# Kernel tuning notes

Hardware: AMD Instinct MI355X
Metric: run time of the kernel (lower is better)

## Reference

```python
import jax, jax.numpy as jnp
import numpy as np

B, F, T, D, S = 8, 256, 512, 40, 4


def setup_inputs() -> dict:
    key = jax.random.key(0)
    k1, k2 = jax.random.split(key)
    embeddings = jax.random.normal(k1, (B, F, T, D), dtype=jnp.float32)
    assignments = jax.random.uniform(k2, (B, F, T, S), dtype=jnp.float32)
    return {"embeddings": embeddings, "assignments": assignments}


def reference(embeddings, assignments):
    b, f, t, d = embeddings.shape
    s = assignments.shape[-1]
    n = f * t
    E = embeddings.reshape(b, n, d)          # (B, N, D)
    V = assignments.reshape(b, n, s)         # (B, N, S)
    # ||VV^T - EE^T||_F^2 summed over batch, via trace identity:
    #   = ||V^T V||_F^2 - 2 ||V^T E||_F^2 + ||E^T E||_F^2
    VtV = jnp.einsum('bns,bnt->bst', V, V)   # (B, S, S)
    VtE = jnp.einsum('bns,bnd->bsd', V, E)   # (B, S, D)
    EtE = jnp.einsum('bnd,bne->bde', E, E)   # (B, D, D)
    fro_sq = jnp.sum(VtV * VtV) - 2.0 * jnp.sum(VtE * VtE) + jnp.sum(EtE * EtE)
    return fro_sq / (b * n)
```

## Files before the change

kernel.cpp:

```cpp
#include <hip/hip_runtime.h>
#include <hip/hip_bf16.h>

#define BATCHES 8
#define NROWS (256 * 512)
#define DE 40
#define SV 4
#define GP 48
#define NTILE 1536
#define ROWS_PER_BLOCK 1024
#define CHUNKS (NROWS / ROWS_PER_BLOCK)
#define RSTAGE 128
#define NSTAGES (ROWS_PER_BLOCK / RSTAGE)
#define COLBYTES 256
#define TILEBYTES (GP * COLBYTES)

typedef __attribute__((ext_vector_type(8))) short bf16x8;
typedef __attribute__((ext_vector_type(4))) float f32x4;
typedef __attribute__((ext_vector_type(2))) int i32x2;
typedef __attribute__((ext_vector_type(4))) float f4v;

__device__ __forceinline__ int pk_bf16(float lo, float hi) {
    __hip_bfloat162 h2 = __float22bfloat162_rn(float2{lo, hi});
    return *reinterpret_cast<int*>(&h2);
}

__device__ __forceinline__ float4 ldnt(const float4* p) {
    f4v v = __builtin_nontemporal_load(reinterpret_cast<const f4v*>(p));
    return make_float4(v.x, v.y, v.z, v.w);
}

__device__ __forceinline__ void bar_lgkm() {
    asm volatile("s_waitcnt lgkmcnt(0)" ::: "memory");
    __builtin_amdgcn_s_barrier();
    asm volatile("" ::: "memory");
}

struct ARegs { float4 a0, a1, a2, a3; };

__global__ __launch_bounds__(256, 4) void gram_kernel(const float* __restrict__ E,
                                                      const float* __restrict__ V,
                                                      float* __restrict__ P) {
    __shared__ __align__(16) char tb[2][TILEBYTES];

    const int tid = threadIdx.x;
    const int lane = tid & 63;
    const int wave = tid >> 6;
    const int b = blockIdx.x / CHUNKS;
    const int chunk = blockIdx.x % CHUNKS;
    const size_t row0 = (size_t)chunk * ROWS_PER_BLOCK;

    const float4* __restrict__ Eg = (const float4*)(E + (size_t)b * NROWS * DE) + row0 * 10;
    const float4* __restrict__ Vg = (const float4*)(V + (size_t)b * NROWS * SV) + row0;

    if (tid < 128) {
        const int bb = tid >> 6, off = (tid & 63) * 16;
        *(float4*)&tb[bb][44 * COLBYTES + off] = make_float4(0.f, 0.f, 0.f, 0.f);
    }

    const int cgA = tid % 11, rgA = tid / 11;
    const int cgB = (tid + 256) % 11, rgB = (tid + 256) / 11;
    const bool hasB = (tid < 96);
    const bool vA = (cgA == 10), vB = (cgB == 10);
    const int pA = vA ? 1 : 10, cA = vA ? 0 : cgA;
    const int pB = vB ? 1 : 10, cB = vB ? 0 : cgB;
    const float4* __restrict__ gA = vA ? Vg : Eg;
    const float4* __restrict__ gB = vB ? Vg : Eg;
    const int oA = 4 * rgA * pA + cA;
    const int oB = 4 * rgB * pB + cB;

    f32x4 acc[6];
    #pragma unroll
    for (int i = 0; i < 6; ++i) acc[i] = (f32x4){0.f, 0.f, 0.f, 0.f};

    const int fcol = lane & 15;
    const int fq = lane >> 4;
    const int fo0 = (wave * 64 + fq * 16 + 16 * ((0 + fcol + (fcol >> 2)) & 15)) & 255;
    const int fo1 = (wave * 64 + fq * 16 + 16 * ((4 + fcol + (fcol >> 2)) & 15)) & 255;
    const int fo2 = (wave * 64 + fq * 16 + 16 * ((8 + fcol + (fcol >> 2)) & 15)) & 255;

    ARegs A[2];
    float4 b0, b1, b2, b3;

    auto load_a = [&](ARegs& r, int sidx) {
        const int adv = sidx * RSTAGE;
        r.a0 = ldnt(&gA[oA + adv * pA]);          r.a1 = ldnt(&gA[oA + adv * pA + pA]);
        r.a2 = ldnt(&gA[oA + adv * pA + 2 * pA]); r.a3 = ldnt(&gA[oA + adv * pA + 3 * pA]);
    };
    auto load_b = [&](int sidx) {
        if (!hasB) return;
        const int adv = sidx * RSTAGE;
        b0 = ldnt(&gB[oB + adv * pB]);          b1 = ldnt(&gB[oB + adv * pB + pB]);
        b2 = ldnt(&gB[oB + adv * pB + 2 * pB]); b3 = ldnt(&gB[oB + adv * pB + 3 * pB]);
    };
    auto write_stage = [&](const ARegs& r, int bufidx) {
        char* base = tb[bufidx];
        #pragma unroll
        for (int j = 0; j < 4; ++j) {
            const float f0 = (j == 0) ? r.a0.x : (j == 1) ? r.a0.y : (j == 2) ? r.a0.z : r.a0.w;
            const float f1 = (j == 0) ? r.a1.x : (j == 1) ? r.a1.y : (j == 2) ? r.a1.z : r.a1.w;
            const float f2 = (j == 0) ? r.a2.x : (j == 1) ? r.a2.y : (j == 2) ? r.a2.z : r.a2.w;
            const float f3 = (j == 0) ? r.a3.x : (j == 1) ? r.a3.y : (j == 2) ? r.a3.z : r.a3.w;
            const int col = 4 * cgA + j;
            const int off = (8 * rgA + 16 * ((5 * cgA + j) & 15)) & 255;
            i32x2 p = { pk_bf16(f0, f1), pk_bf16(f2, f3) };
            *(i32x2*)&base[col * COLBYTES + off] = p;
        }
        if (hasB) {
            #pragma unroll
            for (int j = 0; j < 4; ++j) {
                const float f0 = (j == 0) ? b0.x : (j == 1) ? b0.y : (j == 2) ? b0.z : b0.w;
                const float f1 = (j == 0) ? b1.x : (j == 1) ? b1.y : (j == 2) ? b1.z : b1.w;
                const float f2 = (j == 0) ? b2.x : (j == 1) ? b2.y : (j == 2) ? b2.z : b2.w;
                const float f3 = (j == 0) ? b3.x : (j == 1) ? b3.y : (j == 2) ? b3.z : b3.w;
                const int col = 4 * cgB + j;
                const int off = (8 * rgB + 16 * ((5 * cgB + j) & 15)) & 255;
                i32x2 p = { pk_bf16(f0, f1), pk_bf16(f2, f3) };
                *(i32x2*)&base[col * COLBYTES + off] = p;
            }
        }
    };

    load_a(A[0], 0);
    load_b(0);
    load_a(A[1], 1);
    write_stage(A[0], 0);
    load_b(1);
    load_a(A[0], 2);
    bar_lgkm();

    #pragma unroll
    for (int s = 0; s < NSTAGES; ++s) {
        {
            const char* base = tb[s & 1];
            const bf16x8 f0 = *(const bf16x8*)&base[(0 * 16 + fcol) * COLBYTES + fo0];
            const bf16x8 f1 = *(const bf16x8*)&base[(1 * 16 + fcol) * COLBYTES + fo1];
            const bf16x8 f2 = *(const bf16x8*)&base[(2 * 16 + fcol) * COLBYTES + fo2];
            acc[0] = __builtin_amdgcn_mfma_f32_16x16x32_bf16(f0, f0, acc[0], 0, 0, 0);
            acc[1] = __builtin_amdgcn_mfma_f32_16x16x32_bf16(f1, f0, acc[1], 0, 0, 0);
            acc[2] = __builtin_amdgcn_mfma_f32_16x16x32_bf16(f1, f1, acc[2], 0, 0, 0);
            acc[3] = __builtin_amdgcn_mfma_f32_16x16x32_bf16(f2, f0, acc[3], 0, 0, 0);
            acc[4] = __builtin_amdgcn_mfma_f32_16x16x32_bf16(f2, f1, acc[4], 0, 0, 0);
            acc[5] = __builtin_amdgcn_mfma_f32_16x16x32_bf16(f2, f2, acc[5], 0, 0, 0);
        }
        if (s + 1 < NSTAGES) write_stage(A[(s + 1) & 1], (s + 1) & 1);
        if (s + 3 < NSTAGES) load_a(A[(s + 1) & 1], s + 3);
        if (s + 2 < NSTAGES) load_b(s + 2);
        bar_lgkm();
    }

    float* part = (float*)tb;
    #pragma unroll
    for (int t6 = 0; t6 < 6; ++t6) {
        #pragma unroll
        for (int r = 0; r < 4; ++r)
            part[wave * NTILE + t6 * 256 + (fq * 4 + r) * 16 + fcol] = acc[t6][r];
    }
    bar_lgkm();

    float* __restrict__ Pb = P + (size_t)blockIdx.x * NTILE;
    #pragma unroll
    for (int i = 0; i < 6; ++i) {
        const int e = tid + 256 * i;
        Pb[e] = part[e] + part[NTILE + e] + part[2 * NTILE + e] + part[3 * NTILE + e];
    }
}

__global__ __launch_bounds__(256) void reduce_finish(const float* __restrict__ P,
                                                     float* __restrict__ out) {
    const int tid = threadIdx.x;
    const int b = blockIdx.x / 24;
    const int e0 = (blockIdx.x % 24) * 64;
    const int cs = tid / 64;
    const int el = tid % 64;
    const int e = e0 + el;

    float g = 0.f;
    const float* base = P + (size_t)b * CHUNKS * NTILE + e;
    #pragma unroll 4
    for (int c = cs; c < CHUNKS; c += 4) g += base[(size_t)c * NTILE];

    __shared__ float part[4][64];
    part[cs][el] = g;
    __syncthreads();

    float contrib = 0.f;
    if (tid < 64) {
        g = part[0][el] + part[1][el] + part[2][el] + part[3][el];
        const int t6 = e >> 8;
        const int t = (t6 >= 3) ? 2 : (t6 >= 1) ? 1 : 0;
        const int u = t6 - ((t * (t + 1)) >> 1);
        const int gi = 16 * t + ((e >> 4) & 15);
        const int gj = 16 * u + (e & 15);
        if (gi < (DE + SV) && gj <= gi) {
            const float w = (gi == gj) ? 1.f : 2.f;
            const float sgn = ((gi < DE) == (gj < DE)) ? 1.f : -1.f;
            contrib = w * sgn * g * g;
        }
        #pragma unroll
        for (int o = 32; o > 0; o >>= 1) contrib += __shfl_down(contrib, o, 64);
        if (tid == 0)
            atomicAdd(out, contrib * (1.f / ((float)BATCHES * (float)NROWS)));
    }
}

extern "C" void kernel_launch(void* const* d_in, const int* in_sizes, int n_in,
                              void* d_out, int out_size, void* d_ws, size_t ws_size,
                              hipStream_t stream) {
    const float* E = (const float*)d_in[0];
    const float* V = (const float*)d_in[1];
    float* P = (float*)d_ws;

    (void)hipMemsetAsync(d_out, 0, sizeof(float), stream);
    gram_kernel<<<BATCHES * CHUNKS, 256, 0, stream>>>(E, V, P);
    reduce_finish<<<BATCHES * 24, 256, 0, stream>>>(P, (float*)d_out);
}
```

Measured before the change: 241.2 us.

## Fuse final reduction into gram kernel via atomics and last-block ticket

Each block now atomically adds its partial Gram tile into a per-batch accumulator instead of writing per-chunk partials. A global ticket counter picks the last block to finish, which squares and weights the accumulated Gram entries and writes the final scalar. This drops the second kernel launch and the partial-buffer round trip. In exchange it adds 1536 float atomics per block to shared addresses (128-way contention per batch), a threadfence, and a serialized tail done by one block.

After: 438.2 us. 81.7% more time.

```diff
diff --git a/kernel.cpp b/kernel.cpp
--- a/kernel.cpp
+++ b/kernel.cpp
@@ -13,6 +13,7 @@
 #define NSTAGES (ROWS_PER_BLOCK / RSTAGE)
 #define COLBYTES 256
 #define TILEBYTES (GP * COLBYTES)
+#define GTOT (BATCHES * NTILE)
 
 typedef __attribute__((ext_vector_type(8))) short bf16x8;
 typedef __attribute__((ext_vector_type(4))) float f32x4;
@@ -39,8 +40,12 @@
 
 __global__ __launch_bounds__(256, 4) void gram_kernel(const float* __restrict__ E,
                                                       const float* __restrict__ V,
-                                                      float* __restrict__ P) {
+                                                      float* __restrict__ G,
+                                                      unsigned* __restrict__ ticket,
+                                                      float* __restrict__ out) {
     __shared__ __align__(16) char tb[2][TILEBYTES];
+    __shared__ float red[4];
+    __shared__ unsigned done;
 
     const int tid = threadIdx.x;
     const int lane = tid & 63;
@@ -157,35 +162,32 @@
     }
     bar_lgkm();
 
-    float* __restrict__ Pb = P + (size_t)blockIdx.x * NTILE;
+    float* __restrict__ Gb = G + (size_t)b * NTILE;
     #pragma unroll
     for (int i = 0; i < 6; ++i) {
         const int e = tid + 256 * i;
-        Pb[e] = part[e] + part[NTILE + e] + part[2 * NTILE + e] + part[3 * NTILE + e];
-    }
-}
-
-__global__ __launch_bounds__(256) void reduce_finish(const float* __restrict__ P,
-                                                     float* __restrict__ out) {
-    const int tid = threadIdx.x;
-    const int b = blockIdx.x / 24;
-    const int e0 = (blockIdx.x % 24) * 64;
-    const int cs = tid / 64;
-    const int el = tid % 64;
-    const int e = e0 + el;
-
-    float g = 0.f;
-    const float* base = P + (size_t)b * CHUNKS * NTILE + e;
-    #pragma unroll 4
-    for (int c = cs; c < CHUNKS; c += 4) g += base[(size_t)c * NTILE];
-
-    __shared__ float part[4][64];
-    part[cs][el] = g;
+        const float v = part[e] + part[NTILE + e] + part[2 * NTILE + e] + part[3 * NTILE + e];
+        atomicAdd(&Gb[e], v);
+    }
+
+    __threadfence();
     __syncthreads();
-
-    float contrib = 0.f;
-    if (tid < 64) {
-        g = part[0][el] + part[1][el] + part[2][el] + part[3][el];
+    if (tid == 0)
+        done = __hip_atomic_fetch_add(ticket, 1u, __ATOMIC_ACQ_REL, __HIP_MEMORY_SCOPE_AGENT);
+    __syncthreads();
+    if (done != (unsigned)(gridDim.x - 1)) return;
+
+    float csum = 0.f;
+    #pragma unroll
+    for (int i = 0; i < NTILE / 256; ++i) {
+        const int e = tid + 256 * i;
+        float ss = 0.f;
+        #pragma unroll
+        for (int bb = 0; bb < BATCHES; ++bb) {
+            const float g = __hip_atomic_load(&G[bb * NTILE + e],
+                                              __ATOMIC_RELAXED, __HIP_MEMORY_SCOPE_AGENT);
+            ss += g * g;
+        }
         const int t6 = e >> 8;
         const int t = (t6 >= 3) ? 2 : (t6 >= 1) ? 1 : 0;
         const int u = t6 - ((t * (t + 1)) >> 1);
@@ -194,13 +196,15 @@
         if (gi < (DE + SV) && gj <= gi) {
             const float w = (gi == gj) ? 1.f : 2.f;
             const float sgn = ((gi < DE) == (gj < DE)) ? 1.f : -1.f;
-            contrib = w * sgn * g * g;
-        }
-        #pragma unroll
-        for (int o = 32; o > 0; o >>= 1) contrib += __shfl_down(contrib, o, 64);
-        if (tid == 0)
-            atomicAdd(out, contrib * (1.f / ((float)BATCHES * (float)NROWS)));
-    }
+            csum += w * sgn * ss;
+        }
+    }
+    #pragma unroll
+    for (int o = 32; o > 0; o >>= 1) csum += __shfl_down(csum, o, 64);
+    if (lane == 0) red[wave] = csum;
+    __syncthreads();
+    if (tid == 0)
+        out[0] = (red[0] + red[1] + red[2] + red[3]) * (1.f / ((float)BATCHES * (float)NROWS));
 }
 
 extern "C" void kernel_launch(void* const* d_in, const int* in_sizes, int n_in,
@@ -208,9 +212,9 @@
                               hipStream_t stream) {
     const float* E = (const float*)d_in[0];
     const float* V = (const float*)d_in[1];
-    float* P = (float*)d_ws;
-
-    (void)hipMemsetAsync(d_out, 0, sizeof(float), stream);
-    gram_kernel<<<BATCHES * CHUNKS, 256, 0, stream>>>(E, V, P);
-    reduce_finish<<<BATCHES * 24, 256, 0, stream>>>(P, (float*)d_out);
-}
+    float* G = (float*)d_ws;
+    unsigned* ticket = (unsigned*)((char*)d_ws + GTOT * sizeof(float));
+
+    (void)hipMemsetAsync(d_ws, 0, GTOT * sizeof(float) + sizeof(unsigned), stream);
+    gram_kernel<<<BATCHES * CHUNKS, 256, 0, stream>>>(E, V, G, ticket, (float*)d_out);
+}
```
